# Optimization experiments

Hardware: AMD Instinct MI355X
Metric: run time of the kernel (lower is better)

The kernel has to match this reference:

```python
import jax, jax.numpy as jnp
import numpy as np

D_MODEL = 1024
NUM_HEADS = 16
MAX_LEN = 512  # chunk_size
BATCH = 2
SEQ_LEN = 2048


def _mha(x, w_in, b_in, w_out, b_out, num_heads):
    """torch.nn.MultiheadAttention (eval mode, self-attn) over the last-but-one axis.
    x: (..., S, d). Packed in-proj weight w_in: (3d, d), out-proj w_out: (d, d)."""
    *batch, S, d = x.shape
    hd = d // num_heads
    qkv = x @ w_in.T + b_in                      # (..., S, 3d)
    q, k, v = jnp.split(qkv, 3, axis=-1)
    def heads(t):
        return t.reshape(*batch, S, num_heads, hd)
    q, k, v = heads(q), heads(k), heads(v)
    scale = 1.0 / np.sqrt(hd).astype(np.float32)
    scores = jnp.einsum('...qhd,...khd->...hqk', q, k) * scale
    attn = jax.nn.softmax(scores, axis=-1)
    o = jnp.einsum('...hqk,...khd->...qhd', attn, v).reshape(*batch, S, d)
    return o @ w_out.T + b_out


def setup_inputs() -> dict:
    key = jax.random.key(0)
    ks = jax.random.split(key, 5)
    d = D_MODEL
    s = 0.02
    return {
        'x': jax.random.normal(ks[0], (BATCH, SEQ_LEN, d), dtype=jnp.float32),
        'w_in_l': jax.random.normal(ks[1], (3 * d, d), dtype=jnp.float32) * s,
        'b_in_l': jnp.zeros((3 * d,), jnp.float32),
        'w_out_l': jax.random.normal(ks[2], (d, d), dtype=jnp.float32) * s,
        'b_out_l': jnp.zeros((d,), jnp.float32),
        'w_in_g': jax.random.normal(ks[3], (3 * d, d), dtype=jnp.float32) * s,
        'b_in_g': jnp.zeros((3 * d,), jnp.float32),
        'w_out_g': jax.random.normal(ks[4], (d, d), dtype=jnp.float32) * s,
        'b_out_g': jnp.zeros((d,), jnp.float32),
    }


def reference(x, w_in_l, b_in_l, w_out_l, b_out_l, w_in_g, b_in_g, w_out_g, b_out_g):
    B, S, d = x.shape
    cs = MAX_LEN
    nc = S // cs
    # (B, nc, cs, d) -> (B, cs, nc, d): for each intra-chunk position, attend across chunks.
    xc = x.reshape(B, nc, cs, d).transpose(0, 2, 1, 3)
    # Vectorized replacement for the python loop over chunk positions:
    # batched MHA with batch (B, cs) and sequence length nc.
    loc = _mha(xc, w_in_l, b_in_l, w_out_l, b_out_l, NUM_HEADS)  # (B, cs, nc, d)
    # Faithful to torch: stack -> (nc, cs, B, d), transpose(1,2) -> (nc, B, cs, d),
    # then raw reshape to (B, S, d) (a layout-reinterpreting view, preserved here).
    loc = loc.transpose(2, 0, 1, 3).reshape(B, S, d)
    # Global full self-attention over the whole sequence.
    return _mha(loc, w_in_g, b_in_g, w_out_g, b_out_g, NUM_HEADS)
```

## Files before the change

### kernel.cpp

```cpp
#include <hip/hip_runtime.h>

#define BB 2
#define SS 2048
#define DD 1024
#define HH 16
#define HD 64
#define CS 512
#define NC 4
#define TD 3072
#define MM 4096

typedef __attribute__((ext_vector_type(8))) short short8;
typedef __attribute__((ext_vector_type(4))) float floatx4;
typedef __attribute__((ext_vector_type(2))) unsigned int uintx2;

__device__ __forceinline__ float bf2f(unsigned short h) {
  union { unsigned int u; float f; } v; v.u = ((unsigned int)h) << 16; return v.f;
}
__device__ __forceinline__ unsigned short f2bf(float f) {
  union { float f; unsigned int u; } v; v.f = f;
  unsigned int r = (v.u + 0x7fffu + ((v.u >> 16) & 1u)) >> 16;
  return (unsigned short)r;
}
__device__ __forceinline__ short8 ld8f(const float* p) {
  floatx4 f0 = *(const floatx4*)p;
  floatx4 f1 = *(const floatx4*)(p + 4);
  short8 o;
  o[0] = (short)f2bf(f0[0]); o[1] = (short)f2bf(f0[1]);
  o[2] = (short)f2bf(f0[2]); o[3] = (short)f2bf(f0[3]);
  o[4] = (short)f2bf(f1[0]); o[5] = (short)f2bf(f1[1]);
  o[6] = (short)f2bf(f1[2]); o[7] = (short)f2bf(f1[3]);
  return o;
}
__device__ __forceinline__ short8 scale8_eighth(short8 a) {
  short8 o;
#pragma unroll
  for (int j = 0; j < 8; ++j) o[j] = (short)f2bf(bf2f((unsigned short)a[j]) * 0.125f);
  return o;
}
__device__ __forceinline__ void async16(const void* g, void* l) {
  __builtin_amdgcn_global_load_lds((const __attribute__((address_space(1))) void*)g,
                                   (__attribute__((address_space(3))) void*)l, 16, 0, 0);
}

__global__ __launch_bounds__(256) void cvt_all(
    const float* __restrict__ s0, unsigned short* __restrict__ d0, int n0,
    const float* __restrict__ s1, unsigned short* __restrict__ d1, int n1,
    const float* __restrict__ s2, unsigned short* __restrict__ d2, int n2,
    const float* __restrict__ s3, unsigned short* __restrict__ d3, int n3) {
  int bb = blockIdx.x;
  const float* s; unsigned short* d; int off;
  if (bb < n0) { s = s0; d = d0; off = bb; }
  else if (bb < n0 + n1) { s = s1; d = d1; off = bb - n0; }
  else if (bb < n0 + n1 + n2) { s = s2; d = d2; off = bb - n0 - n1; }
  else { s = s3; d = d3; off = bb - n0 - n1 - n2; }
  int i = (off * 256 + threadIdx.x) * 8;
  *(short8*)(d + i) = ld8f(s + i);
}

__global__ __launch_bounds__(256) void cvt_bf16(const float* __restrict__ in,
                                                unsigned short* __restrict__ out, int n) {
  int i = (blockIdx.x * 256 + threadIdx.x) * 8;
  if (i < n) *(short8*)(out + i) = ld8f(in + i);
}

template <int MT, int C_F32>
__global__ __launch_bounds__(256) void gemm_bt_bias(
    const unsigned short* __restrict__ A, const unsigned short* __restrict__ W,
    const float* __restrict__ bias, void* __restrict__ Cv, int M, int N, int K) {
  constexpr int AI = MT / 32;
  __shared__ unsigned short sA[MT * 64];
  __shared__ unsigned short sB[128 * 64];
  const int tid = threadIdx.x;
  const int wid = tid >> 6, lane = tid & 63;
  const int quad = lane >> 4, l15 = lane & 15;
  const int wm = wid & 1, wn = wid >> 1;
  const int bm = blockIdx.y, bn = blockIdx.x;

  floatx4 acc[AI][4];
#pragma unroll
  for (int i = 0; i < AI; ++i)
#pragma unroll
    for (int j = 0; j < 4; ++j) acc[i][j] = (floatx4){0.f, 0.f, 0.f, 0.f};

  const int rb = tid >> 3;
  const int colsw = ((tid & 7) ^ (rb & 7)) << 3;
  const unsigned short* gA = A + (size_t)(bm * MT + rb) * K + colsw;
  const unsigned short* gW = W + (size_t)(bn * 128 + rb) * K + colsw;
  unsigned short* lA = sA + wid * 512;
  unsigned short* lB = sB + wid * 512;

  for (int k0 = 0; k0 < K; k0 += 64) {
#pragma unroll
    for (int i = 0; i < MT / 32; ++i)
      async16(gA + (size_t)(i * 32) * K + k0, lA + i * 2048);
#pragma unroll
    for (int i = 0; i < 4; ++i)
      async16(gW + (size_t)(i * 32) * K + k0, lB + i * 2048);
    __syncthreads();

#pragma unroll
    for (int kk = 0; kk < 2; ++kk) {
      short8 af[AI], bfr[4];
#pragma unroll
      for (int i = 0; i < AI; ++i) {
        int row = wm * (MT / 2) + i * 16 + l15;
        af[i] = *(const short8*)(sA + row * 64 + ((((kk << 2) | quad) ^ (row & 7)) << 3));
      }
#pragma unroll
      for (int j = 0; j < 4; ++j) {
        int row = wn * 64 + j * 16 + l15;
        bfr[j] = *(const short8*)(sB + row * 64 + ((((kk << 2) | quad) ^ (row & 7)) << 3));
      }
#pragma unroll
      for (int i = 0; i < AI; ++i)
#pragma unroll
        for (int j = 0; j < 4; ++j)
          acc[i][j] = __builtin_amdgcn_mfma_f32_16x16x32_bf16(af[i], bfr[j], acc[i][j], 0, 0, 0);
    }
    __syncthreads();
  }

#pragma unroll
  for (int j = 0; j < 4; ++j) {
    int n = bn * 128 + wn * 64 + j * 16 + l15;
    float bv = bias[n];
#pragma unroll
    for (int i = 0; i < AI; ++i) {
      int mrow = bm * MT + wm * (MT / 2) + i * 16 + quad * 4;
#pragma unroll
      for (int rr = 0; rr < 4; ++rr) {
        float v = acc[i][j][rr] + bv;
        if (C_F32) ((float*)Cv)[(size_t)(mrow + rr) * N + n] = v;
        else ((unsigned short*)Cv)[(size_t)(mrow + rr) * N + n] = f2bf(v);
      }
    }
  }
}

__global__ __launch_bounds__(256) void attn_local(const unsigned short* __restrict__ QKV,
                                                  unsigned short* __restrict__ O) {
  const int tid = threadIdx.x;
  const int wid = tid >> 6, lane = tid & 63;
  const int idx = blockIdx.x * 4 + wid;
  const int h = idx & 15, c = (idx >> 4) & 511, b = idx >> 13;

  float q[NC], k[NC], v[NC];
#pragma unroll
  for (int n = 0; n < NC; ++n) {
    size_t base = (size_t)(b * SS + n * CS + c) * TD + h * HD + lane;
    q[n] = bf2f(QKV[base]);
    k[n] = bf2f(QKV[base + DD]);
    v[n] = bf2f(QKV[base + 2 * DD]);
  }
  float s[NC][NC];
#pragma unroll
  for (int m = 0; m < NC; ++m)
#pragma unroll
    for (int n = 0; n < NC; ++n) {
      float p = q[m] * k[n];
#pragma unroll
      for (int off = 32; off >= 1; off >>= 1) p += __shfl_xor(p, off);
      s[m][n] = p * 0.125f;
    }
#pragma unroll
  for (int m = 0; m < NC; ++m) {
    float mx = fmaxf(fmaxf(s[m][0], s[m][1]), fmaxf(s[m][2], s[m][3]));
    float e[NC], sum = 0.f;
#pragma unroll
    for (int n = 0; n < NC; ++n) { e[n] = __expf(s[m][n] - mx); sum += e[n]; }
    float o = (e[0] * v[0] + e[1] * v[1] + e[2] * v[2] + e[3] * v[3]) / sum;
    O[(size_t)(m * (BB * CS) + b * CS + c) * DD + h * HD + lane] = f2bf(o);
  }
}

__global__ __launch_bounds__(256) void transpose_v(const unsigned short* __restrict__ QKV,
                                                   unsigned short* __restrict__ VT) {
  __shared__ unsigned short sT[64 * 64];
  const int tid = threadIdx.x;
  const int bh = blockIdx.x, b = bh >> 4, h = bh & 15;
  const int s0 = blockIdx.y * 64;
#pragma unroll
  for (int it = 0; it < 2; ++it) {
    int C = it * 256 + tid;
    int t = C >> 3, dc = C & 7;
    short8 v = *(const short8*)(QKV + (size_t)(b * SS + s0 + t) * TD + 2 * DD + h * HD + dc * 8);
    *(short8*)(sT + t * 64 + ((dc ^ (t & 7)) << 3)) = v;
  }
  __syncthreads();
#pragma unroll
  for (int it = 0; it < 2; ++it) {
    int C = it * 256 + tid;
    int d = C >> 3, tc = C & 7;
    short8 o;
#pragma unroll
    for (int j = 0; j < 8; ++j) {
      int t = tc * 8 + j;
      o[j] = (short)sT[t * 64 + (((d >> 3) ^ (t & 7)) << 3) + (d & 7)];
    }
    *(short8*)(VT + ((size_t)(bh * 64 + d)) * SS + s0 + tc * 8) = o;
  }
}

__global__ __launch_bounds__(256, 4) void attn_global(
    const unsigned short* __restrict__ Q, const unsigned short* __restrict__ Kp,
    const unsigned short* __restrict__ VT, unsigned short* __restrict__ O) {
  __shared__ unsigned short sK[2][64 * 64];
  __shared__ unsigned short sVT[2][64 * 64];
  __shared__ float lsb[2][64];
  const int tid = threadIdx.x;
  const int wid = tid >> 6, lane = tid & 63;
  const int quad = lane >> 4, l15 = lane & 15;
  const int qhalf = wid & 1, khalf = wid >> 1;
  const int bh = blockIdx.x;
  const int b = bh >> 4, h = bh & 15;
  const int q0 = blockIdx.y * 64 + qhalf * 32;

  short8 qf[2][2];
#pragma unroll
  for (int g = 0; g < 2; ++g) {
    const unsigned short* qr = Q + (size_t)(b * SS + q0 + g * 16 + l15) * TD + h * HD + quad * 8;
    qf[g][0] = scale8_eighth(*(const short8*)qr);
    qf[g][1] = scale8_eighth(*(const short8*)(qr + 32));
  }

  float lsum[2] = {0.f, 0.f};
  floatx4 oacc[2][4];
#pragma unroll
  for (int g = 0; g < 2; ++g)
#pragma unroll
    for (int s = 0; s < 4; ++s) oacc[g][s] = (floatx4){0.f, 0.f, 0.f, 0.f};

  const unsigned short* myK = &sK[khalf][0];
  const unsigned short* myV = &sVT[khalf][0];
  const unsigned short* vbase = VT + (size_t)(bh * 64) * SS;

  unsigned int koff[2], voff[2];
#pragma unroll
  for (int it = 0; it < 2; ++it) {
    const int P = it * 256 + tid;
    const int row = P >> 3, s = P & 7;
    koff[it] = (unsigned int)((b * SS + row) * TD + h * HD + ((s ^ (row & 7)) << 3));
    voff[it] = (unsigned int)(row * SS + ((s ^ (row & 7)) << 3));
  }

  for (int t = 0; t < 16; ++t) {
#pragma unroll
    for (int kh = 0; kh < 2; ++kh) {
      const int kbase = (kh * 16 + t) * 64;
#pragma unroll
      for (int it = 0; it < 2; ++it) {
        async16(Kp + (size_t)kbase * TD + koff[it], (unsigned short*)&sK[kh][0] + it * 2048 + wid * 512);
        async16(vbase + kbase + voff[it], (unsigned short*)&sVT[kh][0] + it * 2048 + wid * 512);
      }
    }
    __syncthreads();

    floatx4 sacc[2][4];
#pragma unroll
    for (int sub = 0; sub < 4; ++sub) {
      int key = sub * 16 + l15;
      int c0 = (quad ^ (key & 7)) << 3;
      short8 kf0 = *(const short8*)(myK + key * 64 + c0);
      short8 kf1 = *(const short8*)(myK + key * 64 + (c0 ^ 32));
#pragma unroll
      for (int g = 0; g < 2; ++g) {
        floatx4 z = (floatx4){0.f, 0.f, 0.f, 0.f};
        z = __builtin_amdgcn_mfma_f32_16x16x32_bf16(kf0, qf[g][0], z, 0, 0, 0);
        z = __builtin_amdgcn_mfma_f32_16x16x32_bf16(kf1, qf[g][1], z, 0, 0, 0);
        sacc[g][sub] = z;
      }
    }

    short8 pf[2][2];
#pragma unroll
    for (int g = 0; g < 2; ++g)
#pragma unroll
      for (int c = 0; c < 2; ++c) {
        unsigned int w[4];
#pragma unroll
        for (int hs = 0; hs < 2; ++hs) {
          const floatx4 z = sacc[g][2 * c + hs];
          unsigned int u0 = __float_as_uint(__expf(z[0]));
          unsigned int u1 = __float_as_uint(__expf(z[1]));
          unsigned int u2 = __float_as_uint(__expf(z[2]));
          unsigned int u3 = __float_as_uint(__expf(z[3]));
          lsum[g] += __uint_as_float(u0 & 0xffff0000u);
          lsum[g] += __uint_as_float(u1 & 0xffff0000u);
          lsum[g] += __uint_as_float(u2 & 0xffff0000u);
          lsum[g] += __uint_as_float(u3 & 0xffff0000u);
          w[hs * 2 + 0] = (u0 >> 16) | (u1 & 0xffff0000u);
          w[hs * 2 + 1] = (u2 >> 16) | (u3 & 0xffff0000u);
        }
        union { unsigned int u[4]; short8 s; } pk;
        pk.u[0] = w[0]; pk.u[1] = w[1]; pk.u[2] = w[2]; pk.u[3] = w[3];
        pf[g][c] = pk.s;
      }

#pragma unroll
    for (int sub = 0; sub < 4; ++sub) {
      const int n = sub * 16 + l15;
      const int nsw = n & 7;
      const int inner = (quad & 1) * 4;
      short8 vb[2];
#pragma unroll
      for (int c = 0; c < 2; ++c) {
        const int c8a = (((c << 2) | (quad >> 1)) ^ nsw);
        const int c8b = (((c << 2) | 2 | (quad >> 1)) ^ nsw);
        uintx2 a = *(const uintx2*)(myV + n * 64 + c8a * 8 + inner);
        uintx2 d = *(const uintx2*)(myV + n * 64 + c8b * 8 + inner);
        union { unsigned int u[4]; short8 s; } vk;
        vk.u[0] = a[0]; vk.u[1] = a[1]; vk.u[2] = d[0]; vk.u[3] = d[1];
        vb[c] = vk.s;
      }
#pragma unroll
      for (int g = 0; g < 2; ++g) {
        oacc[g][sub] = __builtin_amdgcn_mfma_f32_16x16x32_bf16(pf[g][0], vb[0], oacc[g][sub], 0, 0, 0);
        oacc[g][sub] = __builtin_amdgcn_mfma_f32_16x16x32_bf16(pf[g][1], vb[1], oacc[g][sub], 0, 0, 0);
      }
    }
    __syncthreads();
  }

  float lh[2];
#pragma unroll
  for (int g = 0; g < 2; ++g) {
    float s = lsum[g];
    s += __shfl_xor(s, 16);
    s += __shfl_xor(s, 32);
    lh[g] = s;
  }
  if (lane < 16) {
#pragma unroll
    for (int g = 0; g < 2; ++g) lsb[khalf][qhalf * 32 + g * 16 + l15] = lh[g];
  }

  float* obuf = (float*)&sK[0][0];
  if (khalf == 1) {
    float* my = obuf + qhalf * 2048;
#pragma unroll
    for (int g = 0; g < 2; ++g)
#pragma unroll
      for (int sub = 0; sub < 4; ++sub)
#pragma unroll
        for (int rr = 0; rr < 4; ++rr)
          my[(g * 16 + quad * 4 + rr) * 64 + sub * 16 + l15] = oacc[g][sub][rr];
  }
  __syncthreads();
  if (khalf == 0) {
    float* my = obuf + qhalf * 2048;
#pragma unroll
    for (int g = 0; g < 2; ++g) {
      float inv[4];
#pragma unroll
      for (int rr = 0; rr < 4; ++rr) {
        int idx = qhalf * 32 + g * 16 + quad * 4 + rr;
        inv[rr] = 1.f / (lsb[0][idx] + lsb[1][idx]);
      }
#pragma unroll
      for (int sub = 0; sub < 4; ++sub)
#pragma unroll
        for (int rr = 0; rr < 4; ++rr) {
          float v = oacc[g][sub][rr] + my[(g * 16 + quad * 4 + rr) * 64 + sub * 16 + l15];
          int row = b * SS + q0 + g * 16 + quad * 4 + rr;
          O[(size_t)row * DD + h * HD + sub * 16 + l15] = f2bf(v * inv[rr]);
        }
    }
  }
}

extern "C" void kernel_launch(void* const* d_in, const int* in_sizes, int n_in,
                              void* d_out, int out_size, void* d_ws, size_t ws_size,
                              hipStream_t stream) {
  const float* x       = (const float*)d_in[0];
  const float* w_in_l  = (const float*)d_in[1];
  const float* b_in_l  = (const float*)d_in[2];
  const float* w_out_l = (const float*)d_in[3];
  const float* b_out_l = (const float*)d_in[4];
  const float* w_in_g  = (const float*)d_in[5];
  const float* b_in_g  = (const float*)d_in[6];
  const float* w_out_g = (const float*)d_in[7];
  const float* b_out_g = (const float*)d_in[8];

  unsigned short* wsA = (unsigned short*)d_ws;
  unsigned short* wsB = wsA + (size_t)MM * TD;
  unsigned short* dob = (unsigned short*)d_out;
  unsigned short* wbf_out_l = dob;
  unsigned short* wbf_in_g  = dob + (size_t)DD * DD;
  unsigned short* wbf_in_l  = dob + 4 * (size_t)DD * DD;
  unsigned short* o1        = dob + 4 * (size_t)DD * DD;
  unsigned short* vtbuf     = dob;

  dim3 blk(256);
  cvt_all<<<dim3(5632), blk, 0, stream>>>(w_out_l, wbf_out_l, 512,
                                          w_in_g, wbf_in_g, 1536,
                                          w_in_l, wbf_in_l, 1536,
                                          x, wsB, 2048);

  gemm_bt_bias<128, 0><<<dim3(TD / 128, MM / 128), blk, 0, stream>>>(wsB, wbf_in_l, b_in_l, wsA, MM, TD, DD);
  attn_local<<<dim3(BB * CS * HH / 4), blk, 0, stream>>>(wsA, o1);
  gemm_bt_bias<64, 0><<<dim3(DD / 128, MM / 64), blk, 0, stream>>>(o1, wbf_out_l, b_out_l, wsB, MM, DD, DD);
  gemm_bt_bias<128, 0><<<dim3(TD / 128, MM / 128), blk, 0, stream>>>(wsB, wbf_in_g, b_in_g, wsA, MM, TD, DD);
  transpose_v<<<dim3(BB * HH, SS / 64), blk, 0, stream>>>(wsA, vtbuf);
  attn_global<<<dim3(BB * HH, SS / 64), blk, 0, stream>>>(wsA, wsA + DD, vtbuf, wsB);
  cvt_bf16<<<dim3(DD * DD / 2048), blk, 0, stream>>>(w_out_g, wsA, DD * DD);
  gemm_bt_bias<64, 1><<<dim3(DD / 128, MM / 64), blk, 0, stream>>>(wsB, wsA, b_out_g, d_out, MM, DD, DD);
}
```

Measured before the change: 298.7 us.

## Drop split-K waves in global attention; use 128-thread blocks over full key range

The global attention kernel previously used 4 waves, with two query halves times two key halves, and merged the key-half partial outputs and softmax sums through shared memory. It now uses 2 waves per block, each covering 32 queries across all 32 key tiles, and normalizes directly from registers using a shuffle of the row sums. This removes the cross-wave reduction, the extra barrier and half the shared memory. In exchange each block runs twice as many serial key iterations with fewer waves to hide load latency.

```diff
diff --git a/kernel.cpp b/kernel.cpp
--- a/kernel.cpp
+++ b/kernel.cpp
@@ -202,19 +202,17 @@
   }
 }
 
-__global__ __launch_bounds__(256, 4) void attn_global(
+__global__ __launch_bounds__(128, 5) void attn_global(
     const unsigned short* __restrict__ Q, const unsigned short* __restrict__ Kp,
     const unsigned short* __restrict__ VT, unsigned short* __restrict__ O) {
-  __shared__ unsigned short sK[2][64 * 64];
-  __shared__ unsigned short sVT[2][64 * 64];
-  __shared__ float lsb[2][64];
+  __shared__ unsigned short sK[64 * 64];
+  __shared__ unsigned short sVT[64 * 64];
   const int tid = threadIdx.x;
   const int wid = tid >> 6, lane = tid & 63;
   const int quad = lane >> 4, l15 = lane & 15;
-  const int qhalf = wid & 1, khalf = wid >> 1;
   const int bh = blockIdx.x;
   const int b = bh >> 4, h = bh & 15;
-  const int q0 = blockIdx.y * 64 + qhalf * 32;
+  const int q0 = blockIdx.y * 64 + wid * 32;
 
   short8 qf[2][2];
 #pragma unroll
@@ -231,29 +229,25 @@
 #pragma unroll
     for (int s = 0; s < 4; ++s) oacc[g][s] = (floatx4){0.f, 0.f, 0.f, 0.f};
 
-  const unsigned short* myK = &sK[khalf][0];
-  const unsigned short* myV = &sVT[khalf][0];
   const unsigned short* vbase = VT + (size_t)(bh * 64) * SS;
 
-  unsigned int koff[2], voff[2];
-#pragma unroll
-  for (int it = 0; it < 2; ++it) {
-    const int P = it * 256 + tid;
+  unsigned int koff[4], voff[4];
+#pragma unroll
+  for (int it = 0; it < 4; ++it) {
+    const int P = it * 128 + tid;
     const int row = P >> 3, s = P & 7;
     koff[it] = (unsigned int)((b * SS + row) * TD + h * HD + ((s ^ (row & 7)) << 3));
     voff[it] = (unsigned int)(row * SS + ((s ^ (row & 7)) << 3));
   }
 
-  for (int t = 0; t < 16; ++t) {
-#pragma unroll
-    for (int kh = 0; kh < 2; ++kh) {
-      const int kbase = (kh * 16 + t) * 64;
-#pragma unroll
-      for (int it = 0; it < 2; ++it) {
-        async16(Kp + (size_t)kbase * TD + koff[it], (unsigned short*)&sK[kh][0] + it * 2048 + wid * 512);
-        async16(vbase + kbase + voff[it], (unsigned short*)&sVT[kh][0] + it * 2048 + wid * 512);
-      }
-    }
+  for (int t = 0; t < 32; ++t) {
+    const int kbase = t * 64;
+#pragma unroll
+    for (int it = 0; it < 4; ++it)
+      async16(Kp + (size_t)kbase * TD + koff[it], (unsigned short*)sK + it * 1024 + wid * 512);
+#pragma unroll
+    for (int it = 0; it < 4; ++it)
+      async16(vbase + kbase + voff[it], (unsigned short*)sVT + it * 1024 + wid * 512);
     __syncthreads();
 
     floatx4 sacc[2][4];
@@ -261,8 +255,8 @@
     for (int sub = 0; sub < 4; ++sub) {
       int key = sub * 16 + l15;
       int c0 = (quad ^ (key & 7)) << 3;
-      short8 kf0 = *(const short8*)(myK + key * 64 + c0);
-      short8 kf1 = *(const short8*)(myK + key * 64 + (c0 ^ 32));
+      short8 kf0 = *(const short8*)(sK + key * 64 + c0);
+      short8 kf1 = *(const short8*)(sK + key * 64 + (c0 ^ 32));
 #pragma unroll
       for (int g = 0; g < 2; ++g) {
         floatx4 z = (floatx4){0.f, 0.f, 0.f, 0.f};
@@ -307,8 +301,8 @@
       for (int c = 0; c < 2; ++c) {
         const int c8a = (((c << 2) | (quad >> 1)) ^ nsw);
         const int c8b = (((c << 2) | 2 | (quad >> 1)) ^ nsw);
-        uintx2 a = *(const uintx2*)(myV + n * 64 + c8a * 8 + inner);
-        uintx2 d = *(const uintx2*)(myV + n * 64 + c8b * 8 + inner);
+        uintx2 a = *(const uintx2*)(sVT + n * 64 + c8a * 8 + inner);
+        uintx2 d = *(const uintx2*)(sVT + n * 64 + c8b * 8 + inner);
         union { unsigned int u[4]; short8 s; } vk;
         vk.u[0] = a[0]; vk.u[1] = a[1]; vk.u[2] = d[0]; vk.u[3] = d[1];
         vb[c] = vk.s;
@@ -330,42 +324,18 @@
     s += __shfl_xor(s, 32);
     lh[g] = s;
   }
-  if (lane < 16) {
-#pragma unroll
-    for (int g = 0; g < 2; ++g) lsb[khalf][qhalf * 32 + g * 16 + l15] = lh[g];
-  }
-
-  float* obuf = (float*)&sK[0][0];
-  if (khalf == 1) {
-    float* my = obuf + qhalf * 2048;
-#pragma unroll
-    for (int g = 0; g < 2; ++g)
-#pragma unroll
-      for (int sub = 0; sub < 4; ++sub)
-#pragma unroll
-        for (int rr = 0; rr < 4; ++rr)
-          my[(g * 16 + quad * 4 + rr) * 64 + sub * 16 + l15] = oacc[g][sub][rr];
-  }
-  __syncthreads();
-  if (khalf == 0) {
-    float* my = obuf + qhalf * 2048;
-#pragma unroll
-    for (int g = 0; g < 2; ++g) {
-      float inv[4];
+#pragma unroll
+  for (int g = 0; g < 2; ++g) {
+    float inv[4];
+#pragma unroll
+    for (int rr = 0; rr < 4; ++rr) inv[rr] = 1.f / __shfl(lh[g], quad * 4 + rr);
+#pragma unroll
+    for (int sub = 0; sub < 4; ++sub)
 #pragma unroll
       for (int rr = 0; rr < 4; ++rr) {
-        int idx = qhalf * 32 + g * 16 + quad * 4 + rr;
-        inv[rr] = 1.f / (lsb[0][idx] + lsb[1][idx]);
-      }
-#pragma unroll
-      for (int sub = 0; sub < 4; ++sub)
-#pragma unroll
-        for (int rr = 0; rr < 4; ++rr) {
-          float v = oacc[g][sub][rr] + my[(g * 16 + quad * 4 + rr) * 64 + sub * 16 + l15];
-          int row = b * SS + q0 + g * 16 + quad * 4 + rr;
-          O[(size_t)row * DD + h * HD + sub * 16 + l15] = f2bf(v * inv[rr]);
-        }
-    }
+        int row = b * SS + q0 + g * 16 + quad * 4 + rr;
+        O[(size_t)row * DD + h * HD + sub * 16 + l15] = f2bf(oacc[g][sub][rr] * inv[rr]);
+      }
   }
 }
 
@@ -402,7 +372,7 @@
   gemm_bt_bias<64, 0><<<dim3(DD / 128, MM / 64), blk, 0, stream>>>(o1, wbf_out_l, b_out_l, wsB, MM, DD, DD);
   gemm_bt_bias<128, 0><<<dim3(TD / 128, MM / 128), blk, 0, stream>>>(wsB, wbf_in_g, b_in_g, wsA, MM, TD, DD);
   transpose_v<<<dim3(BB * HH, SS / 64), blk, 0, stream>>>(wsA, vtbuf);
-  attn_global<<<dim3(BB * HH, SS / 64), blk, 0, stream>>>(wsA, wsA + DD, vtbuf, wsB);
+  attn_global<<<dim3(BB * HH, SS / 64), dim3(128), 0, stream>>>(wsA, wsA + DD, vtbuf, wsB);
   cvt_bf16<<<dim3(DD * DD / 2048), blk, 0, stream>>>(w_out_g, wsA, DD * DD);
   gemm_bt_bias<64, 1><<<dim3(DD / 128, MM / 64), blk, 0, stream>>>(wsB, wsA, b_out_g, d_out, MM, DD, DD);
 }
```

Result: slower. 382.7 us (+28.1%).
